# Optimization experiments

Hardware: AMD Instinct MI355X
Metric: run time of the kernel (lower is better)

## Reference

```python
import jax, jax.numpy as jnp
import numpy as np

B, C, H, W = 4, 256, 64, 64
CQK = C // 2


def setup_inputs() -> dict:
    key = jax.random.key(0)
    ks = jax.random.split(key, 8)
    s = 0.05
    return {
        "x": jax.random.normal(ks[0], (B, C, H, W), dtype=jnp.float32),
        "wq": jax.random.normal(ks[1], (CQK, C), dtype=jnp.float32) * s,
        "bq": jax.random.normal(ks[2], (CQK,), dtype=jnp.float32) * s,
        "wk": jax.random.normal(ks[3], (CQK, C), dtype=jnp.float32) * s,
        "bk": jax.random.normal(ks[4], (CQK,), dtype=jnp.float32) * s,
        "wv": jax.random.normal(ks[5], (C, C), dtype=jnp.float32) * s,
        "bv": jax.random.normal(ks[6], (C,), dtype=jnp.float32) * s,
        "gamma": jax.random.normal(ks[7], (1,), dtype=jnp.float32),
    }


def reference(x, wq, bq, wk, bk, wv, bv, gamma):
    b, c, h, w = x.shape
    n = h * w
    xf = x.reshape(b, c, n)  # [B,C,N]
    # 1x1 convs == per-pixel linear projections
    q = jnp.einsum("oc,bcn->bon", wq, xf) + bq[:, None]  # [B,C/2,N]
    k = jnp.einsum("oc,bcn->bon", wk, xf) + bk[:, None]  # [B,C/2,N]
    v = jnp.einsum("oc,bcn->bon", wv, xf) + bv[:, None]  # [B,C,N]
    # attention[b,m,n'] = softmax_n'( sum_d q[b,d,m] * k[b,d,n'] )
    scores = jnp.einsum("bdm,bdn->bmn", q, k)  # [B,N,N]
    attn = jax.nn.softmax(scores, axis=2)
    # out_feat[b,c,j] = sum_i v[b,c,i] * attn[b,i,j]  (matmul(value, attention))
    af = jnp.einsum("bci,bij->bcj", v, attn)  # [B,C,N]
    out = gamma[0] * af.reshape(b, c, h, w) + x
    return out
```

## Files before the change

### kernel.cpp

```cpp
#include <hip/hip_runtime.h>
#include <hip/hip_bf16.h>


typedef _Float16 f16;
typedef _Float16 f16x4v __attribute__((ext_vector_type(4)));
typedef _Float16 f16x8v __attribute__((ext_vector_type(8)));
typedef float f32x4v __attribute__((ext_vector_type(4)));

static __device__ __forceinline__ f32x4v mfma16(f16x8v a, f16x8v b, f32x4v c) {
  return __builtin_amdgcn_mfma_f32_16x16x32_f16(a, b, c, 0, 0, 0);
}

__global__ void k_xsplit(const float* __restrict__ x, f16* __restrict__ xh,
                         const float* __restrict__ wq, const float* __restrict__ bq,
                         const float* __restrict__ wk, const float* __restrict__ bk,
                         const float* __restrict__ wv, const float* __restrict__ bv,
                         f16* __restrict__ wh, float* __restrict__ bcat) {
  int id = blockIdx.x + 64 * (blockIdx.y + 4 * blockIdx.z);
  if (id < 512) {
    int o = id, c = threadIdx.x;
    const float* wrow; float bias;
    if (o < 128)      { wrow = wq + (size_t)o * 256;         bias = bq[o]; }
    else if (o < 256) { wrow = wk + (size_t)(o - 128) * 256; bias = bk[o - 128]; }
    else              { wrow = wv + (size_t)(o - 256) * 256; bias = bv[o - 256]; }
    wh[(size_t)(o >> 4) * 4096 + (size_t)(c >> 5) * 512 +
       (size_t)((c >> 3) & 3) * 128 + (o & 15) * 8 + (c & 7)] = (f16)wrow[c];
    if (c == 0) bcat[o] = bias;
  }
  __shared__ float t[64][65];
  int b = blockIdx.z, c0 = blockIdx.y * 64, n0 = blockIdx.x * 64;
  int tx = threadIdx.x & 63, ty = threadIdx.x >> 6;
  const float* xb = x + ((size_t)b * 256 + c0) * 4096 + n0;
#pragma unroll
  for (int r = ty; r < 64; r += 4) t[r][tx] = xb[(size_t)r * 4096 + tx];
  __syncthreads();
  f16* xbb = xh + (size_t)b * 1048576;
#pragma unroll
  for (int k2 = 0; k2 < 2; k2++) {
    int id2 = k2 * 256 + threadIdx.x;
    int tok = id2 & 63, oct = id2 >> 6;
    int tt = n0 + tok;
    f16x8v v;
#pragma unroll
    for (int e = 0; e < 8; e++) v[e] = (f16)t[oct * 8 + e][tok];
    size_t addr = (size_t)(tt >> 4) * 4096 +
                  (size_t)((c0 >> 5) + (oct >> 2)) * 512 +
                  (size_t)(oct & 3) * 128 + (tt & 15) * 8;
    *(f16x8v*)&xbb[addr] = v;
  }
}

__global__ void __launch_bounds__(512, 1)
k_proj(const f16* __restrict__ xh, const f16* __restrict__ wh,
       const float* __restrict__ bcat, f16* __restrict__ qT,
       f16* __restrict__ kT, f16* __restrict__ vT) {
  int ob = blockIdx.x, th = blockIdx.y, b = blockIdx.z;
  int tid = threadIdx.x, l = tid & 63, w = tid >> 6;
  int col = l & 15, quad = l >> 4;
  int tt = w & 3, oh = w >> 2;
  int OT0 = ob * 4 + oh * 2;
  const f16* wtb = wh + (size_t)OT0 * 4096 + l * 8;
  f16x8v wb[2][8];
#pragma unroll
  for (int jt = 0; jt < 2; jt++)
#pragma unroll
    for (int ks = 0; ks < 8; ks++)
      wb[jt][ks] = *(const f16x8v*)(wtb + jt * 4096 + ks * 512);
  float bias0 = bcat[OT0 * 16 + col];
  float bias1 = bcat[OT0 * 16 + 16 + col];
  const f16* atb = xh + (size_t)b * 1048576 + (size_t)(th * 32 + tt) * 4096 + l * 8;
  f16x8v afA[8], afB[8];
#pragma unroll
  for (int ks = 0; ks < 8; ks++) afA[ks] = *(const f16x8v*)(atb + ks * 512);

#define PROJ_BODY(IT, AF, AN, PREF)                                            \
  {                                                                            \
    if (PREF) {                                                                \
      _Pragma("unroll") for (int ks = 0; ks < 8; ks++)                         \
        AN[ks] = *(const f16x8v*)(atb + (size_t)((IT) + 1) * 16384 + ks * 512);\
    }                                                                          \
    f32x4v s0 = {}, s1 = {};                                                   \
    _Pragma("unroll") for (int ks = 0; ks < 8; ks++) {                         \
      s0 = mfma16(AF[ks], wb[0][ks], s0);                                      \
      s1 = mfma16(AF[ks], wb[1][ks], s1);                                      \
    }                                                                          \
    int T = th * 32 + (IT) * 4 + tt;                                           \
    if (ob < 4) {                                                              \
      f16* dst = (ob < 2) ? qT : kT;                                           \
      _Pragma("unroll") for (int jt = 0; jt < 2; jt++) {                       \
        int o = OT0 * 16 + jt * 16 + col;                                      \
        int d = o & 127;                                                       \
        float bs = jt ? bias1 : bias0;                                         \
        size_t base = (size_t)b * 524288 + (size_t)T * 2048 +                  \
                      (size_t)(d >> 5) * 512 + (size_t)((d >> 3) & 3) * 128 +  \
                      (d & 7);                                                 \
        float sv0 = jt ? s1[0] : s0[0], sv1 = jt ? s1[1] : s0[1];              \
        float sv2 = jt ? s1[2] : s0[2], sv3 = jt ? s1[3] : s0[3];              \
        dst[base + (quad * 4 + 0) * 8] = (f16)(sv0 + bs);                      \
        dst[base + (quad * 4 + 1) * 8] = (f16)(sv1 + bs);                      \
        dst[base + (quad * 4 + 2) * 8] = (f16)(sv2 + bs);                      \
        dst[base + (quad * 4 + 3) * 8] = (f16)(sv3 + bs);                      \
      }                                                                        \
    } else {                                                                   \
      int i0 = T * 16 + quad * 4;                                              \
      size_t ibase = (size_t)b * 1048576 + (size_t)(i0 >> 5) * 512 +           \
                     (size_t)((i0 >> 3) & 3) * 128 + (i0 & 7);                 \
      _Pragma("unroll") for (int jt = 0; jt < 2; jt++) {                       \
        int c = OT0 * 16 + jt * 16 + col - 256;                                \
        float bs = jt ? bias1 : bias0;                                         \
        f16x4v pv;                                                             \
        _Pragma("unroll") for (int rg = 0; rg < 4; rg++)                       \
          pv[rg] = (f16)((jt ? s1[rg] : s0[rg]) + bs);                         \
        *(f16x4v*)&vT[ibase + (size_t)(c >> 4) * 65536 + (c & 15) * 8] = pv;   \
      }                                                                        \
    }                                                                          \
  }

  for (int itp = 0; itp < 4; itp++) {
    int itA = itp * 2;
    PROJ_BODY(itA, afA, afB, true)
    PROJ_BODY(itA + 1, afB, afA, itp < 3)
  }
#undef PROJ_BODY
}

__global__ void __launch_bounds__(512, 2)
k_rows(const f16* __restrict__ qT, const f16* __restrict__ kT,
       float* __restrict__ partial) {
  int jblk = blockIdx.x, ih = blockIdx.y, b = blockIdx.z;
  int tid = threadIdx.x, l = tid & 63, w = tid >> 6;
  int col = l & 15;
  int ti = w & 3, jh = w >> 2;
  const f16* ktb = kT + (size_t)b * 524288 + (size_t)(jblk * 8 + jh * 4) * 2048 + l * 8;
  const f16* qtb = qT + (size_t)b * 524288 + (size_t)ti * 2048 + l * 8;
  f16x8v ka[4][4];
#pragma unroll
  for (int jt = 0; jt < 4; jt++)
#pragma unroll
    for (int ks = 0; ks < 4; ks++)
      ka[jt][ks] = *(const f16x8v*)(ktb + jt * 2048 + ks * 512);
  float* pout = partial + ((size_t)(b * 32 + jblk) * 2 + jh) * 4096 + ti * 16 + col;
  int it0 = ih * 32;
  f16x8v qfA[4], qfB[4];
#pragma unroll
  for (int ks = 0; ks < 4; ks++)
    qfA[ks] = *(const f16x8v*)(qtb + (size_t)it0 * 8192 + ks * 512);

#define ROWS_BODY(IT, QF, QN, PREF)                                           \
  {                                                                           \
    if (PREF) {                                                               \
      _Pragma("unroll") for (int ks = 0; ks < 4; ks++)                        \
        QN[ks] = *(const f16x8v*)(qtb + (size_t)((IT) + 1) * 8192 + ks * 512);\
    }                                                                         \
    f32x4v s[4] = {};                                                         \
    _Pragma("unroll") for (int ks = 0; ks < 4; ks++) {                        \
      s[0] = mfma16(ka[0][ks], QF[ks], s[0]);                                 \
      s[1] = mfma16(ka[1][ks], QF[ks], s[1]);                                 \
      s[2] = mfma16(ka[2][ks], QF[ks], s[2]);                                 \
      s[3] = mfma16(ka[3][ks], QF[ks], s[3]);                                 \
    }                                                                         \
    float t = 0.f;                                                            \
    _Pragma("unroll") for (int jt = 0; jt < 4; jt++)                          \
      _Pragma("unroll") for (int rg = 0; rg < 4; rg++)                        \
        t += __expf(s[jt][rg]);                                               \
    t += __shfl_xor(t, 16);                                                   \
    t += __shfl_xor(t, 32);                                                   \
    if (l < 16) pout[(size_t)(IT) * 64] = t;                                  \
  }

  for (int itp = 0; itp < 16; itp++) {
    int itA = it0 + itp * 2;
    ROWS_BODY(itA, qfA, qfB, true)
    ROWS_BODY(itA + 1, qfB, qfA, itp < 15)
  }
#undef ROWS_BODY
}

__global__ void k_rsum(const float* __restrict__ partial, float* __restrict__ rinv) {
  int b = blockIdx.y;
  int i = blockIdx.x * 256 + threadIdx.x;
  const float* p = partial + (size_t)b * 64 * 4096 + i;
  float s = 0.f;
#pragma unroll 8
  for (int jb = 0; jb < 64; jb++) s += p[(size_t)jb * 4096];
  rinv[(size_t)b * 4096 + i] = 1.0f / s;
}

__global__ void __launch_bounds__(512, 1)
k_fav(const f16* __restrict__ qT, const f16* __restrict__ kT,
      const f16* __restrict__ vT, const float* __restrict__ rinv,
      const float* __restrict__ x, const float* __restrict__ gamma,
      float* __restrict__ out) {
  __shared__ f16 sE[2][2][4096];
  int wg = blockIdx.x;
  int lg = (wg & 7) * 32 + (wg >> 3);
  int b = lg >> 6, j0 = (lg & 63) * 64;
  int tid = threadIdx.x, l = tid & 63, w = tid >> 6;
  int col = l & 15, quad = l >> 4;
  int ti = w & 3, sel = w >> 2;
  const f16* ktb = kT + (size_t)b * 524288 + (size_t)(j0 / 16) * 2048 + l * 8;
  const f16* qtb = qT + (size_t)b * 524288 + (size_t)ti * 2048 + l * 8;
  const f16* vtb = vT + (size_t)b * 1048576 + (size_t)(w * 2) * 65536 + l * 8;
  const float* rp = rinv + (size_t)b * 4096 + ti * 16 + col;
  f16x8v ka[4][4];
#pragma unroll
  for (int jt = 0; jt < 4; jt++)
#pragma unroll
    for (int ks = 0; ks < 4; ks++)
      ka[jt][ks] = *(const f16x8v*)(ktb + jt * 2048 + ks * 512);
  f16x8v qf[4], vfA[2][2], vfB[2][2];
#pragma unroll
  for (int ks = 0; ks < 4; ks++)
    qf[ks] = *(const f16x8v*)(qtb + (size_t)sel * 8192 + ks * 512);
  float rv = rp[sel * 64];
  f32x4v acc[2][4] = {};
  int ig = ti * 2 + (col >> 3);
  int i_lo = col & 7;

#define FAV_WR(SJ, JT, P)                                                      \
  _Pragma("unroll") for (int rg = 0; rg < 4; rg++) {                           \
    int jl = (JT) * 16 + quad * 4 + rg;                                        \
    sE[P][sel][jl * 64 + ((ig ^ (jl & 7)) * 8) + i_lo] =                       \
        (f16)(__expf(SJ[rg]) * rv);                                            \
  }

#define FAV_AV(VF, P, SET)                                                     \
  {                                                                            \
    _Pragma("unroll") for (int ks = 0; ks < 2; ks++) {                         \
      int sw = ((ks * 4 + quad) ^ (col & 7)) * 8;                              \
      f16x8v e0 = *(const f16x8v*)&sE[P][SET][col * 64 + sw];                  \
      f16x8v e1 = *(const f16x8v*)&sE[P][SET][(16 + col) * 64 + sw];           \
      f16x8v e2 = *(const f16x8v*)&sE[P][SET][(32 + col) * 64 + sw];           \
      f16x8v e3 = *(const f16x8v*)&sE[P][SET][(48 + col) * 64 + sw];           \
      acc[0][0] = mfma16(VF[0][ks], e0, acc[0][0]);                            \
      acc[0][1] = mfma16(VF[0][ks], e1, acc[0][1]);                            \
      acc[0][2] = mfma16(VF[0][ks], e2, acc[0][2]);                            \
      acc[0][3] = mfma16(VF[0][ks], e3, acc[0][3]);                            \
      acc[1][0] = mfma16(VF[1][ks], e0, acc[1][0]);                            \
      acc[1][1] = mfma16(VF[1][ks], e1, acc[1][1]);                            \
      acc[1][2] = mfma16(VF[1][ks], e2, acc[1][2]);                            \
      acc[1][3] = mfma16(VF[1][ks], e3, acc[1][3]);                            \
    }                                                                          \
  }

  for (int s = 0; s < 32; s++) {
    int t0 = s * 2;
    int p = s & 1;
#pragma unroll
    for (int mt = 0; mt < 2; mt++)
#pragma unroll
      for (int ks = 0; ks < 2; ks++)
        vfA[mt][ks] = *(const f16x8v*)(vtb + mt * 65536 + (size_t)(t0 * 2 + ks) * 512);
    f32x4v sj0 = {}, sj1 = {}, sj2 = {}, sj3 = {};
#pragma unroll
    for (int ks = 0; ks < 4; ks++) {
      sj0 = mfma16(ka[0][ks], qf[ks], sj0);
      sj1 = mfma16(ka[1][ks], qf[ks], sj1);
      sj2 = mfma16(ka[2][ks], qf[ks], sj2);
      sj3 = mfma16(ka[3][ks], qf[ks], sj3);
    }
#pragma unroll
    for (int mt = 0; mt < 2; mt++)
#pragma unroll
      for (int ks = 0; ks < 2; ks++)
        vfB[mt][ks] = *(const f16x8v*)(vtb + mt * 65536 + (size_t)(t0 * 2 + 2 + ks) * 512);
    if (p) { FAV_WR(sj0, 0, 1) FAV_WR(sj1, 1, 1) FAV_WR(sj2, 2, 1) FAV_WR(sj3, 3, 1) }
    else   { FAV_WR(sj0, 0, 0) FAV_WR(sj1, 1, 0) FAV_WR(sj2, 2, 0) FAV_WR(sj3, 3, 0) }
    asm volatile("s_waitcnt lgkmcnt(0)\n\ts_barrier" ::: "memory");
    if (s < 31) {
#pragma unroll
      for (int ks = 0; ks < 4; ks++)
        qf[ks] = *(const f16x8v*)(qtb + (size_t)(t0 + 2 + sel) * 8192 + ks * 512);
      rv = rp[(size_t)(t0 + 2 + sel) * 64];
    }
    if (p) { FAV_AV(vfA, 1, 0) FAV_AV(vfB, 1, 1) }
    else   { FAV_AV(vfA, 0, 0) FAV_AV(vfB, 0, 1) }
  }
#undef FAV_WR
#undef FAV_AV

  float gm = gamma[0];
  const float* xb = x + (size_t)b * 256 * 4096;
  float* ob = out + (size_t)b * 256 * 4096;
#pragma unroll
  for (int mt = 0; mt < 2; mt++)
#pragma unroll
    for (int jt = 0; jt < 4; jt++) {
      int c = w * 32 + mt * 16 + quad * 4;
      int j = j0 + jt * 16 + col;
#pragma unroll
      for (int rg = 0; rg < 4; rg++) {
        size_t off = (size_t)(c + rg) * 4096 + j;
        ob[off] = gm * acc[mt][jt][rg] + xb[off];
      }
    }
}

extern "C" void kernel_launch(void* const* d_in, const int* in_sizes, int n_in,
                              void* d_out, int out_size, void* d_ws, size_t ws_size,
                              hipStream_t stream) {
  (void)in_sizes; (void)n_in; (void)out_size; (void)ws_size;
  const float* x  = (const float*)d_in[0];
  const float* wq = (const float*)d_in[1];
  const float* bq = (const float*)d_in[2];
  const float* wk = (const float*)d_in[3];
  const float* bk = (const float*)d_in[4];
  const float* wv = (const float*)d_in[5];
  const float* bv = (const float*)d_in[6];
  const float* gm = (const float*)d_in[7];
  float* out = (float*)d_out;

  char* ws = (char*)d_ws;
  f16*  xh = (f16*)ws;
  f16*  qT = (f16*)(ws + 8388608);
  f16*  kT = (f16*)(ws + 12582912);
  f16*  vT = (f16*)(ws + 16777216);
  f16*  wh = (f16*)(ws + 25165824);
  float* bcat    = (float*)(ws + 25427968);
  float* rinv    = (float*)(ws + 25430016);
  float* partial = (float*)(ws + 25495552);

  hipLaunchKernelGGL(k_xsplit, dim3(64, 4, 4), dim3(256), 0, stream,
                     x, xh, wq, bq, wk, bk, wv, bv, wh, bcat);
  hipLaunchKernelGGL(k_proj, dim3(8, 8, 4), dim3(512), 0, stream, xh, wh, bcat, qT, kT, vT);
  hipLaunchKernelGGL(k_rows, dim3(32, 2, 4), dim3(512), 0, stream, qT, kT, partial);
  hipLaunchKernelGGL(k_rsum, dim3(16, 4), dim3(256), 0, stream, partial, rinv);
  hipLaunchKernelGGL(k_fav, dim3(256), dim3(512), 0, stream, qT, kT, vT, rinv, x, gm, out);
}
```

Measured before the change: 174.3 us.

## Split fused attention-V kernel into producer and consumer waves

```diff
diff --git a/kernel.cpp b/kernel.cpp
--- a/kernel.cpp
+++ b/kernel.cpp
@@ -191,109 +191,128 @@
       const f16* __restrict__ vT, const float* __restrict__ rinv,
       const float* __restrict__ x, const float* __restrict__ gamma,
       float* __restrict__ out) {
-  __shared__ f16 sE[2][2][4096];
+  __shared__ f16 sE[2][4096];
   int wg = blockIdx.x;
   int lg = (wg & 7) * 32 + (wg >> 3);
   int b = lg >> 6, j0 = (lg & 63) * 64;
   int tid = threadIdx.x, l = tid & 63, w = tid >> 6;
   int col = l & 15, quad = l >> 4;
-  int ti = w & 3, sel = w >> 2;
-  const f16* ktb = kT + (size_t)b * 524288 + (size_t)(j0 / 16) * 2048 + l * 8;
-  const f16* qtb = qT + (size_t)b * 524288 + (size_t)ti * 2048 + l * 8;
-  const f16* vtb = vT + (size_t)b * 1048576 + (size_t)(w * 2) * 65536 + l * 8;
-  const float* rp = rinv + (size_t)b * 4096 + ti * 16 + col;
-  f16x8v ka[4][4];
-#pragma unroll
-  for (int jt = 0; jt < 4; jt++)
-#pragma unroll
-    for (int ks = 0; ks < 4; ks++)
-      ka[jt][ks] = *(const f16x8v*)(ktb + jt * 2048 + ks * 512);
-  f16x8v qf[4], vfA[2][2], vfB[2][2];
-#pragma unroll
-  for (int ks = 0; ks < 4; ks++)
-    qf[ks] = *(const f16x8v*)(qtb + (size_t)sel * 8192 + ks * 512);
-  float rv = rp[sel * 64];
-  f32x4v acc[2][4] = {};
+  bool prod = (w < 4);
+  int ti = w & 3;
+  int cw = w & 3;
   int ig = ti * 2 + (col >> 3);
   int i_lo = col & 7;
 
-#define FAV_WR(SJ, JT, P)                                                      \
+  const f16* qtb = qT + (size_t)b * 524288 + (size_t)ti * 2048 + l * 8;
+  const f16* ktb = kT + (size_t)b * 524288 + (size_t)(j0 / 16) * 2048 + l * 8;
+  const f16* vtb = vT + (size_t)b * 1048576 + (size_t)(cw * 4) * 65536 + l * 8;
+  const float* rp = rinv + (size_t)b * 4096 + ti * 16 + col;
+
+  f16x8v ka[4][4], qf[4], vf[4][2];
+  f32x4v acc[4][4] = {};
+  float rv = 0.f;
+
+#define FAV_WR(SJ, JT, BUF)                                                    \
   _Pragma("unroll") for (int rg = 0; rg < 4; rg++) {                           \
     int jl = (JT) * 16 + quad * 4 + rg;                                        \
-    sE[P][sel][jl * 64 + ((ig ^ (jl & 7)) * 8) + i_lo] =                       \
+    sE[BUF][jl * 64 + ((ig ^ (jl & 7)) * 8) + i_lo] =                          \
         (f16)(__expf(SJ[rg]) * rv);                                            \
   }
 
-#define FAV_AV(VF, P, SET)                                                     \
+#define FAV_QKW(BUF)                                                           \
   {                                                                            \
-    _Pragma("unroll") for (int ks = 0; ks < 2; ks++) {                         \
-      int sw = ((ks * 4 + quad) ^ (col & 7)) * 8;                              \
-      f16x8v e0 = *(const f16x8v*)&sE[P][SET][col * 64 + sw];                  \
-      f16x8v e1 = *(const f16x8v*)&sE[P][SET][(16 + col) * 64 + sw];           \
-      f16x8v e2 = *(const f16x8v*)&sE[P][SET][(32 + col) * 64 + sw];           \
-      f16x8v e3 = *(const f16x8v*)&sE[P][SET][(48 + col) * 64 + sw];           \
-      acc[0][0] = mfma16(VF[0][ks], e0, acc[0][0]);                            \
-      acc[0][1] = mfma16(VF[0][ks], e1, acc[0][1]);                            \
-      acc[0][2] = mfma16(VF[0][ks], e2, acc[0][2]);                            \
-      acc[0][3] = mfma16(VF[0][ks], e3, acc[0][3]);                            \
-      acc[1][0] = mfma16(VF[1][ks], e0, acc[1][0]);                            \
-      acc[1][1] = mfma16(VF[1][ks], e1, acc[1][1]);                            \
-      acc[1][2] = mfma16(VF[1][ks], e2, acc[1][2]);                            \
-      acc[1][3] = mfma16(VF[1][ks], e3, acc[1][3]);                            \
+    f32x4v sj0 = {}, sj1 = {}, sj2 = {}, sj3 = {};                             \
+    _Pragma("unroll") for (int ks = 0; ks < 4; ks++) {                         \
+      sj0 = mfma16(ka[0][ks], qf[ks], sj0);                                    \
+      sj1 = mfma16(ka[1][ks], qf[ks], sj1);                                    \
+      sj2 = mfma16(ka[2][ks], qf[ks], sj2);                                    \
+      sj3 = mfma16(ka[3][ks], qf[ks], sj3);                                    \
     }                                                                          \
-  }
-
-  for (int s = 0; s < 32; s++) {
-    int t0 = s * 2;
-    int p = s & 1;
-#pragma unroll
-    for (int mt = 0; mt < 2; mt++)
+    FAV_WR(sj0, 0, BUF) FAV_WR(sj1, 1, BUF)                                    \
+    FAV_WR(sj2, 2, BUF) FAV_WR(sj3, 3, BUF)                                    \
+  }
+
+  if (prod) {
+#pragma unroll
+    for (int jt = 0; jt < 4; jt++)
+#pragma unroll
+      for (int ks = 0; ks < 4; ks++)
+        ka[jt][ks] = *(const f16x8v*)(ktb + jt * 2048 + ks * 512);
+#pragma unroll
+    for (int ks = 0; ks < 4; ks++)
+      qf[ks] = *(const f16x8v*)(qtb + ks * 512);
+    rv = rp[0];
+    FAV_QKW(0)
+#pragma unroll
+    for (int ks = 0; ks < 4; ks++)
+      qf[ks] = *(const f16x8v*)(qtb + 8192 + ks * 512);
+    rv = rp[64];
+  } else {
+#pragma unroll
+    for (int mt = 0; mt < 4; mt++)
 #pragma unroll
       for (int ks = 0; ks < 2; ks++)
-        vfA[mt][ks] = *(const f16x8v*)(vtb + mt * 65536 + (size_t)(t0 * 2 + ks) * 512);
-    f32x4v sj0 = {}, sj1 = {}, sj2 = {}, sj3 = {};
-#pragma unroll
-    for (int ks = 0; ks < 4; ks++) {
-      sj0 = mfma16(ka[0][ks], qf[ks], sj0);
-      sj1 = mfma16(ka[1][ks], qf[ks], sj1);
-      sj2 = mfma16(ka[2][ks], qf[ks], sj2);
-      sj3 = mfma16(ka[3][ks], qf[ks], sj3);
+        vf[mt][ks] = *(const f16x8v*)(vtb + mt * 65536 + ks * 512);
+  }
+  asm volatile("s_waitcnt lgkmcnt(0)\n\ts_barrier" ::: "memory");
+
+  for (int t = 0; t < 64; t++) {
+    int p = t & 1;
+    if (prod) {
+      if (t < 63) {
+        if (p) { FAV_QKW(0) } else { FAV_QKW(1) }
+        int tn = t + 2 > 63 ? 63 : t + 2;
+#pragma unroll
+        for (int ks = 0; ks < 4; ks++)
+          qf[ks] = *(const f16x8v*)(qtb + (size_t)tn * 8192 + ks * 512);
+        rv = rp[(size_t)tn * 64];
+      }
+    } else {
+#pragma unroll
+      for (int ks = 0; ks < 2; ks++) {
+        int sw = ((ks * 4 + quad) ^ (col & 7)) * 8;
+        f16x8v e0 = *(const f16x8v*)&sE[p][col * 64 + sw];
+        f16x8v e1 = *(const f16x8v*)&sE[p][(16 + col) * 64 + sw];
+        f16x8v e2 = *(const f16x8v*)&sE[p][(32 + col) * 64 + sw];
+        f16x8v e3 = *(const f16x8v*)&sE[p][(48 + col) * 64 + sw];
+#pragma unroll
+        for (int mt = 0; mt < 4; mt++) {
+          acc[mt][0] = mfma16(vf[mt][ks], e0, acc[mt][0]);
+          acc[mt][1] = mfma16(vf[mt][ks], e1, acc[mt][1]);
+          acc[mt][2] = mfma16(vf[mt][ks], e2, acc[mt][2]);
+          acc[mt][3] = mfma16(vf[mt][ks], e3, acc[mt][3]);
+        }
+      }
+      int tn = t + 1 > 63 ? 63 : t + 1;
+#pragma unroll
+      for (int mt = 0; mt < 4; mt++)
+#pragma unroll
+        for (int ks = 0; ks < 2; ks++)
+          vf[mt][ks] = *(const f16x8v*)(vtb + mt * 65536 +
+                                        (size_t)(tn * 2 + ks) * 512);
     }
-#pragma unroll
-    for (int mt = 0; mt < 2; mt++)
-#pragma unroll
-      for (int ks = 0; ks < 2; ks++)
-        vfB[mt][ks] = *(const f16x8v*)(vtb + mt * 65536 + (size_t)(t0 * 2 + 2 + ks) * 512);
-    if (p) { FAV_WR(sj0, 0, 1) FAV_WR(sj1, 1, 1) FAV_WR(sj2, 2, 1) FAV_WR(sj3, 3, 1) }
-    else   { FAV_WR(sj0, 0, 0) FAV_WR(sj1, 1, 0) FAV_WR(sj2, 2, 0) FAV_WR(sj3, 3, 0) }
     asm volatile("s_waitcnt lgkmcnt(0)\n\ts_barrier" ::: "memory");
-    if (s < 31) {
-#pragma unroll
-      for (int ks = 0; ks < 4; ks++)
-        qf[ks] = *(const f16x8v*)(qtb + (size_t)(t0 + 2 + sel) * 8192 + ks * 512);
-      rv = rp[(size_t)(t0 + 2 + sel) * 64];
-    }
-    if (p) { FAV_AV(vfA, 1, 0) FAV_AV(vfB, 1, 1) }
-    else   { FAV_AV(vfA, 0, 0) FAV_AV(vfB, 0, 1) }
-  }
+  }
+#undef FAV_QKW
 #undef FAV_WR
-#undef FAV_AV
-
-  float gm = gamma[0];
-  const float* xb = x + (size_t)b * 256 * 4096;
-  float* ob = out + (size_t)b * 256 * 4096;
-#pragma unroll
-  for (int mt = 0; mt < 2; mt++)
-#pragma unroll
-    for (int jt = 0; jt < 4; jt++) {
-      int c = w * 32 + mt * 16 + quad * 4;
-      int j = j0 + jt * 16 + col;
-#pragma unroll
-      for (int rg = 0; rg < 4; rg++) {
-        size_t off = (size_t)(c + rg) * 4096 + j;
-        ob[off] = gm * acc[mt][jt][rg] + xb[off];
+
+  if (!prod) {
+    float gm = gamma[0];
+    const float* xb = x + (size_t)b * 256 * 4096;
+    float* ob = out + (size_t)b * 256 * 4096;
+#pragma unroll
+    for (int mt = 0; mt < 4; mt++)
+#pragma unroll
+      for (int jt = 0; jt < 4; jt++) {
+        int c = cw * 64 + mt * 16 + quad * 4;
+        int j = j0 + jt * 16 + col;
+#pragma unroll
+        for (int rg = 0; rg < 4; rg++) {
+          size_t off = (size_t)(c + rg) * 4096 + j;
+          ob[off] = gm * acc[mt][jt][rg] + xb[off];
+        }
       }
-    }
+  }
 }
 
 extern "C" void kernel_launch(void* const* d_in, const int* in_sizes, int n_in,
```

Result: slower. 181.6 us (+4.2%).

## Split attention-value reduction over two i-halves and combine partials separately

Applied to the files above, without the earlier changes.

```diff
diff --git a/kernel.cpp b/kernel.cpp
--- a/kernel.cpp
+++ b/kernel.cpp
@@ -186,22 +186,26 @@
   rinv[(size_t)b * 4096 + i] = 1.0f / s;
 }
 
-__global__ void __launch_bounds__(512, 1)
+__global__ void __launch_bounds__(512, 2)
 k_fav(const f16* __restrict__ qT, const f16* __restrict__ kT,
       const f16* __restrict__ vT, const float* __restrict__ rinv,
-      const float* __restrict__ x, const float* __restrict__ gamma,
-      float* __restrict__ out) {
+      float* __restrict__ pacc) {
   __shared__ f16 sE[2][2][4096];
   int wg = blockIdx.x;
-  int lg = (wg & 7) * 32 + (wg >> 3);
-  int b = lg >> 6, j0 = (lg & 63) * 64;
+  int lg = (wg & 7) * 64 + (wg >> 3);
+  int b = lg >> 7;
+  int rem = lg & 127;
+  int j0 = (rem >> 1) * 64;
+  int ih = rem & 1;
   int tid = threadIdx.x, l = tid & 63, w = tid >> 6;
   int col = l & 15, quad = l >> 4;
   int ti = w & 3, sel = w >> 2;
   const f16* ktb = kT + (size_t)b * 524288 + (size_t)(j0 / 16) * 2048 + l * 8;
-  const f16* qtb = qT + (size_t)b * 524288 + (size_t)ti * 2048 + l * 8;
-  const f16* vtb = vT + (size_t)b * 1048576 + (size_t)(w * 2) * 65536 + l * 8;
-  const float* rp = rinv + (size_t)b * 4096 + ti * 16 + col;
+  const f16* qtb = qT + (size_t)b * 524288 + (size_t)(ih * 32) * 8192 +
+                   (size_t)ti * 2048 + l * 8;
+  const f16* vtb = vT + (size_t)b * 1048576 + (size_t)(w * 2) * 65536 +
+                   (size_t)(ih * 32) * 1024 + l * 8;
+  const float* rp = rinv + (size_t)b * 4096 + ih * 2048 + ti * 16 + col;
   f16x8v ka[4][4];
 #pragma unroll
   for (int jt = 0; jt < 4; jt++)
@@ -243,7 +247,7 @@
     }                                                                          \
   }
 
-  for (int s = 0; s < 32; s++) {
+  for (int s = 0; s < 16; s++) {
     int t0 = s * 2;
     int p = s & 1;
 #pragma unroll
@@ -267,7 +271,7 @@
     if (p) { FAV_WR(sj0, 0, 1) FAV_WR(sj1, 1, 1) FAV_WR(sj2, 2, 1) FAV_WR(sj3, 3, 1) }
     else   { FAV_WR(sj0, 0, 0) FAV_WR(sj1, 1, 0) FAV_WR(sj2, 2, 0) FAV_WR(sj3, 3, 0) }
     asm volatile("s_waitcnt lgkmcnt(0)\n\ts_barrier" ::: "memory");
-    if (s < 31) {
+    if (s < 15) {
 #pragma unroll
       for (int ks = 0; ks < 4; ks++)
         qf[ks] = *(const f16x8v*)(qtb + (size_t)(t0 + 2 + sel) * 8192 + ks * 512);
@@ -279,9 +283,7 @@
 #undef FAV_WR
 #undef FAV_AV
 
-  float gm = gamma[0];
-  const float* xb = x + (size_t)b * 256 * 4096;
-  float* ob = out + (size_t)b * 256 * 4096;
+  float* pD = pacc + (size_t)(ih * 4 + b) * 1048576;
 #pragma unroll
   for (int mt = 0; mt < 2; mt++)
 #pragma unroll
@@ -289,11 +291,22 @@
       int c = w * 32 + mt * 16 + quad * 4;
       int j = j0 + jt * 16 + col;
 #pragma unroll
-      for (int rg = 0; rg < 4; rg++) {
-        size_t off = (size_t)(c + rg) * 4096 + j;
-        ob[off] = gm * acc[mt][jt][rg] + xb[off];
-      }
+      for (int rg = 0; rg < 4; rg++)
+        pD[(size_t)(c + rg) * 4096 + j] = acc[mt][jt][rg];
     }
+}
+
+__global__ void k_comb(const float* __restrict__ pacc, const float* __restrict__ x,
+                       const float* __restrict__ gamma, float* __restrict__ out) {
+  size_t f = ((size_t)blockIdx.x * 256 + threadIdx.x) * 4;
+  float gm = gamma[0];
+  f32x4v a = *(const f32x4v*)&pacc[f];
+  f32x4v bb = *(const f32x4v*)&pacc[4194304 + f];
+  f32x4v xv = *(const f32x4v*)&x[f];
+  f32x4v o;
+#pragma unroll
+  for (int e = 0; e < 4; e++) o[e] = gm * (a[e] + bb[e]) + xv[e];
+  *(f32x4v*)&out[f] = o;
 }
 
 extern "C" void kernel_launch(void* const* d_in, const int* in_sizes, int n_in,
@@ -319,11 +332,13 @@
   float* bcat    = (float*)(ws + 25427968);
   float* rinv    = (float*)(ws + 25430016);
   float* partial = (float*)(ws + 25495552);
+  float* pacc    = (float*)(ws + 33554432);
 
   hipLaunchKernelGGL(k_xsplit, dim3(64, 4, 4), dim3(256), 0, stream,
                      x, xh, wq, bq, wk, bk, wv, bv, wh, bcat);
   hipLaunchKernelGGL(k_proj, dim3(8, 8, 4), dim3(512), 0, stream, xh, wh, bcat, qT, kT, vT);
   hipLaunchKernelGGL(k_rows, dim3(32, 2, 4), dim3(512), 0, stream, qT, kT, partial);
   hipLaunchKernelGGL(k_rsum, dim3(16, 4), dim3(256), 0, stream, partial, rinv);
-  hipLaunchKernelGGL(k_fav, dim3(256), dim3(512), 0, stream, qT, kT, vT, rinv, x, gm, out);
-}
+  hipLaunchKernelGGL(k_fav, dim3(512), dim3(512), 0, stream, qT, kT, vT, rinv, pacc);
+  hipLaunchKernelGGL(k_comb, dim3(4096), dim3(256), 0, stream, pacc, x, gm, out);
+}
```

Result: slower. 183.0 us (+5.0%).
